# Optimization experiments

Hardware: AMD Instinct MI355X
Metric: run time of the kernel (lower is better)

## Reference

```python
import jax, jax.numpy as jnp
import numpy as np


def log_g(x):
    # log of g(x) = x+0.5 if x>=0 else sigmoid(x), computed stably
    return jnp.where(x >= 0, jnp.log(jax.nn.relu(x) + 0.5), -jax.nn.softplus(-x))


def setup_inputs() -> dict:
    key = jax.random.key(0)
    ks = jax.random.split(key, 6)
    B, S, D, H = 8, 4096, 1024, 1024
    scale = 1.0 / np.sqrt(D)
    return {
        "x": jax.random.normal(ks[0], (B, S, D), dtype=jnp.float32),
        "h0": jax.random.normal(ks[1], (B, 1, H), dtype=jnp.float32),
        "Wz": jax.random.normal(ks[2], (H, D), dtype=jnp.float32) * scale,
        "bz": jax.random.normal(ks[3], (H,), dtype=jnp.float32) * scale,
        "Wh": jax.random.normal(ks[4], (H, D), dtype=jnp.float32) * scale,
        "bh": jax.random.normal(ks[5], (H,), dtype=jnp.float32) * scale,
    }


def reference(x, h0, Wz, bz, Wh, bh):
    # x: (B,S,D), h0: (B,1,H)
    k = jnp.einsum("bsd,hd->bsh", x, Wz) + bz            # linear_z
    log_z = -jax.nn.softplus(-k)                          # log sigmoid(k)
    log_coeffs = -jax.nn.softplus(k)                      # log (1 - sigmoid(k))
    log_h0 = log_g(h0)                                    # (B,1,H)
    log_tilde_h = log_g(jnp.einsum("bsd,hd->bsh", x, Wh) + bh)
    log_values = jnp.concatenate([log_h0, log_z + log_tilde_h], axis=1)  # (B,S+1,H)
    a_star = jnp.pad(jnp.cumsum(log_coeffs, axis=1), ((0, 0), (1, 0), (0, 0)))  # (B,S+1,H)
    log_h0_plus_b_star = jax.lax.cumlogsumexp(log_values - a_star, axis=1)
    h = jnp.exp(a_star[:, 1:] + log_h0_plus_b_star[:, 1:])  # (B,S,H)
    return h
```

## Files before the change

### kernel.cpp

```cpp
#include <hip/hip_runtime.h>
#include <cstdint>
#include <cstddef>

#define B_  8
#define S_  4096
#define D_  1024
#define H_  1024
#define M_  (B_*S_)
#define NC_ 64
#define L_  (S_/NC_)

typedef __bf16 bf16x8 __attribute__((ext_vector_type(8)));
typedef float  f32x4  __attribute__((ext_vector_type(4)));
typedef uint16_t u16x8 __attribute__((ext_vector_type(8)));

__device__ __forceinline__ uint16_t f2bf(float f) {
  union { float f; uint32_t u; } v; v.f = f;
  uint32_t u = v.u;
  u += 0x7FFFu + ((u >> 16) & 1u);
  return (uint16_t)(u >> 16);
}
__device__ __forceinline__ float gfun(float x) {
  return x >= 0.0f ? x + 0.5f
                   : __builtin_amdgcn_rcpf(1.0f + __expf(-x));
}
__device__ __forceinline__ void unpack_cv(uint32_t u, float& c, float& v) {
  union { uint32_t u; _Float16 h[2]; } p; p.u = u;
  c = (float)p.h[0]; v = (float)p.h[1];
}

__global__ __launch_bounds__(256) void cvt_kernel(const float* __restrict__ in,
                                                  uint16_t* __restrict__ out,
                                                  int n8) {
  int i = blockIdx.x * 256 + threadIdx.x;
  if (i >= n8) return;
  const float4* p = (const float4*)in;
  float4 a = p[2 * i], b = p[2 * i + 1];
  u16x8 v;
  v[0] = f2bf(a.x); v[1] = f2bf(a.y); v[2] = f2bf(a.z); v[3] = f2bf(a.w);
  v[4] = f2bf(b.x); v[5] = f2bf(b.y); v[6] = f2bf(b.z); v[7] = f2bf(b.w);
  *(u16x8*)&out[8 * i] = v;
}

#define BM 128
#define BNH 64
#define BK 64
__global__ __launch_bounds__(256)
void fused_gemm_kernel(const uint16_t* __restrict__ A,
                       const uint16_t* __restrict__ Wz,
                       const uint16_t* __restrict__ Wh,
                       const float* __restrict__ bz,
                       const float* __restrict__ bh,
                       uint32_t* __restrict__ cv) {
  __shared__ __attribute__((aligned(16))) uint16_t As[BM * BK];
  __shared__ __attribute__((aligned(16))) uint16_t Bzs[BNH * BK];
  __shared__ __attribute__((aligned(16))) uint16_t Bhs[BNH * BK];
  const int tid  = threadIdx.x;
  const int lane = tid & 63;
  const int wave = tid >> 6;
  const int mTile = blockIdx.y * BM;
  const int nTile = blockIdx.x * BNH;
  const int wm0 = (wave >> 1) * 64;
  const int wn0 = (wave & 1) * 32;
  const int q  = lane >> 4;
  const int mn = lane & 15;

  f32x4 accK[4][2] = {};
  f32x4 accP[4][2] = {};

  for (int kt = 0; kt < D_; kt += BK) {
    __syncthreads();
    #pragma unroll
    for (int i = 0; i < 4; i++) {
      int u = i * 256 + tid;
      int r = u >> 3;
      int c = (u & 7) ^ (r & 7);
      __builtin_amdgcn_global_load_lds(
          (const __attribute__((address_space(1))) void*)(A + (size_t)(mTile + r) * D_ + kt + c * 8),
          (__attribute__((address_space(3))) void*)&As[(i * 256 + wave * 64) * 8],
          16, 0, 0);
    }
    #pragma unroll
    for (int i = 0; i < 2; i++) {
      int u = i * 256 + tid;
      int r = u >> 3;
      int c = (u & 7) ^ (r & 7);
      __builtin_amdgcn_global_load_lds(
          (const __attribute__((address_space(1))) void*)(Wz + (size_t)(nTile + r) * D_ + kt + c * 8),
          (__attribute__((address_space(3))) void*)&Bzs[(i * 256 + wave * 64) * 8],
          16, 0, 0);
    }
    #pragma unroll
    for (int i = 0; i < 2; i++) {
      int u = i * 256 + tid;
      int r = u >> 3;
      int c = (u & 7) ^ (r & 7);
      __builtin_amdgcn_global_load_lds(
          (const __attribute__((address_space(1))) void*)(Wh + (size_t)(nTile + r) * D_ + kt + c * 8),
          (__attribute__((address_space(3))) void*)&Bhs[(i * 256 + wave * 64) * 8],
          16, 0, 0);
    }
    __syncthreads();

    #pragma unroll
    for (int s = 0; s < 2; s++) {
      bf16x8 av[4], bzv[2], bhv[2];
      const int cu = s * 4 + q;
      #pragma unroll
      for (int tm = 0; tm < 4; tm++) {
        int r = wm0 + tm * 16 + mn;
        av[tm] = *(const bf16x8*)&As[(r * 8 + (cu ^ (r & 7))) * 8];
      }
      #pragma unroll
      for (int tn = 0; tn < 2; tn++) {
        int r = wn0 + tn * 16 + mn;
        int unit = r * 8 + (cu ^ (r & 7));
        bzv[tn] = *(const bf16x8*)&Bzs[unit * 8];
        bhv[tn] = *(const bf16x8*)&Bhs[unit * 8];
      }
      #pragma unroll
      for (int tm = 0; tm < 4; tm++)
        #pragma unroll
        for (int tn = 0; tn < 2; tn++) {
          accK[tm][tn] = __builtin_amdgcn_mfma_f32_16x16x32_bf16(
              av[tm], bzv[tn], accK[tm][tn], 0, 0, 0);
          accP[tm][tn] = __builtin_amdgcn_mfma_f32_16x16x32_bf16(
              av[tm], bhv[tn], accP[tm][tn], 0, 0, 0);
        }
    }
  }

  #pragma unroll
  for (int tn = 0; tn < 2; tn++) {
    int col = nTile + wn0 + tn * 16 + mn;
    float bzc = bz[col], bhc = bh[col];
    #pragma unroll
    for (int tm = 0; tm < 4; tm++) {
      int row0 = mTile + wm0 + tm * 16 + q * 4;
      #pragma unroll
      for (int i = 0; i < 4; i++) {
        float kv = accK[tm][tn][i] + bzc;
        float pv = accP[tm][tn][i] + bhc;
        float c = __builtin_amdgcn_rcpf(1.0f + __expf(kv));
        float z = 1.0f - c;
        float v = z * gfun(pv);
        union { _Float16 h[2]; uint32_t u; } pk;
        pk.h[0] = (_Float16)c; pk.h[1] = (_Float16)v;
        cv[(size_t)(row0 + i) * H_ + col] = pk.u;
      }
    }
  }
}

__global__ __launch_bounds__(256) void scan_chunk_kernel(
    const uint32_t* __restrict__ cv, float4* __restrict__ Cc,
    float4* __restrict__ Vc) {
  const int tid = threadIdx.x;
  const int nc = blockIdx.x, b = blockIdx.y;
  const uint4* cv4 = (const uint4*)cv;
  size_t base = (size_t)(b * S_ + nc * L_) * (H_ / 4) + tid;
  float C[4] = {1.f, 1.f, 1.f, 1.f};
  float V[4] = {0.f, 0.f, 0.f, 0.f};
  #pragma unroll 4
  for (int t = 0; t < L_; t++) {
    uint4 w = cv4[base + (size_t)t * (H_ / 4)];
    float c, v;
    unpack_cv(w.x, c, v); C[0] *= c; V[0] = c * V[0] + v;
    unpack_cv(w.y, c, v); C[1] *= c; V[1] = c * V[1] + v;
    unpack_cv(w.z, c, v); C[2] *= c; V[2] = c * V[2] + v;
    unpack_cv(w.w, c, v); C[3] *= c; V[3] = c * V[3] + v;
  }
  size_t o = (size_t)(b * NC_ + nc) * (H_ / 4) + tid;
  Cc[o] = (float4){C[0], C[1], C[2], C[3]};
  Vc[o] = (float4){V[0], V[1], V[2], V[3]};
}

__global__ __launch_bounds__(256) void chunk_prefix_kernel(
    const float* __restrict__ Cc, const float* __restrict__ Vc,
    const float* __restrict__ h0, float* __restrict__ Hin) {
  int h = blockIdx.x * 256 + threadIdx.x;
  int b = blockIdx.y;
  float Hv = gfun(h0[(size_t)b * H_ + h]);
  Hin[(size_t)(b * NC_) * H_ + h] = Hv;
  #pragma unroll 8
  for (int nc = 1; nc < NC_; nc++) {
    size_t idx = (size_t)(b * NC_ + nc - 1) * H_ + h;
    Hv = Cc[idx] * Hv + Vc[idx];
    Hin[(size_t)(b * NC_ + nc) * H_ + h] = Hv;
  }
}

__global__ __launch_bounds__(256) void scan_apply_kernel(
    const uint32_t* __restrict__ cv, const float4* __restrict__ Hin,
    float4* __restrict__ out) {
  const int tid = threadIdx.x;
  const int nc = blockIdx.x, b = blockIdx.y;
  const uint4* cv4 = (const uint4*)cv;
  size_t base = (size_t)(b * S_ + nc * L_) * (H_ / 4) + tid;
  float4 Hq = Hin[(size_t)(b * NC_ + nc) * (H_ / 4) + tid];
  float Hr[4] = {Hq.x, Hq.y, Hq.z, Hq.w};
  #pragma unroll 4
  for (int t = 0; t < L_; t++) {
    size_t idx = base + (size_t)t * (H_ / 4);
    uint4 w = cv4[idx];
    float c, v;
    unpack_cv(w.x, c, v); Hr[0] = c * Hr[0] + v;
    unpack_cv(w.y, c, v); Hr[1] = c * Hr[1] + v;
    unpack_cv(w.z, c, v); Hr[2] = c * Hr[2] + v;
    unpack_cv(w.w, c, v); Hr[3] = c * Hr[3] + v;
    out[idx] = (float4){Hr[0], Hr[1], Hr[2], Hr[3]};
  }
}

extern "C" void kernel_launch(void* const* d_in, const int* in_sizes, int n_in,
                              void* d_out, int out_size, void* d_ws, size_t ws_size,
                              hipStream_t stream) {
  const float* x  = (const float*)d_in[0];
  const float* h0 = (const float*)d_in[1];
  const float* Wz = (const float*)d_in[2];
  const float* bz = (const float*)d_in[3];
  const float* Wh = (const float*)d_in[4];
  const float* bh = (const float*)d_in[5];
  float* out = (float*)d_out;

  char* ws = (char*)d_ws;
  uint16_t* xb  = (uint16_t*)ws; ws += (size_t)M_ * D_ * 2;
  uint16_t* Wzb = (uint16_t*)ws; ws += (size_t)H_ * D_ * 2;
  uint16_t* Whb = (uint16_t*)ws; ws += (size_t)H_ * D_ * 2;
  uint32_t* cvb = (uint32_t*)ws; ws += (size_t)M_ * H_ * 4;
  char* alias = (char*)xb;
  float* Cc  = (float*)alias; alias += (size_t)B_ * NC_ * H_ * 4;
  float* Vc  = (float*)alias; alias += (size_t)B_ * NC_ * H_ * 4;
  float* Hin = (float*)alias; alias += (size_t)B_ * NC_ * H_ * 4;

  cvt_kernel<<<dim3(M_ * D_ / 8 / 256), 256, 0, stream>>>(x, xb, M_ * D_ / 8);
  cvt_kernel<<<dim3(H_ * D_ / 8 / 256), 256, 0, stream>>>(Wz, Wzb, H_ * D_ / 8);
  cvt_kernel<<<dim3(H_ * D_ / 8 / 256), 256, 0, stream>>>(Wh, Whb, H_ * D_ / 8);

  fused_gemm_kernel<<<dim3(H_ / BNH, M_ / BM), 256, 0, stream>>>(
      xb, Wzb, Whb, bz, bh, cvb);

  scan_chunk_kernel<<<dim3(NC_, B_), 256, 0, stream>>>(cvb, (float4*)Cc, (float4*)Vc);
  chunk_prefix_kernel<<<dim3(H_ / 256, B_), 256, 0, stream>>>(Cc, Vc, h0, Hin);
  scan_apply_kernel<<<dim3(NC_, B_), 256, 0, stream>>>(cvb, (const float4*)Hin, (float4*)out);
}
```

Measured before the change: 481.7 us.

## Enlarge GEMM N tile, merge conversion kernels, fold chunk prefix into apply

The GEMM tile width per block doubles to 128 columns, so each wave computes 4x4 MFMA tiles for both weight matrices, with precomputed load pointers and a two-blocks-per-CU launch bound. The goal is more reuse of each loaded A tile and fewer blocks. The three fp32-to-bf16 conversion launches become one grid-stride kernel. The serial chunk-prefix kernel is removed and each apply block recomputes its own incoming state from the chunk summaries, trading redundant prefix work for one fewer launch and no Hin buffer. The larger accumulator set raises register pressure and may lower occupancy.

```diff
diff --git a/kernel.cpp b/kernel.cpp
--- a/kernel.cpp
+++ b/kernel.cpp
@@ -29,23 +29,31 @@
   c = (float)p.h[0]; v = (float)p.h[1];
 }
 
-__global__ __launch_bounds__(256) void cvt_kernel(const float* __restrict__ in,
-                                                  uint16_t* __restrict__ out,
-                                                  int n8) {
-  int i = blockIdx.x * 256 + threadIdx.x;
-  if (i >= n8) return;
-  const float4* p = (const float4*)in;
-  float4 a = p[2 * i], b = p[2 * i + 1];
-  u16x8 v;
-  v[0] = f2bf(a.x); v[1] = f2bf(a.y); v[2] = f2bf(a.z); v[3] = f2bf(a.w);
-  v[4] = f2bf(b.x); v[5] = f2bf(b.y); v[6] = f2bf(b.z); v[7] = f2bf(b.w);
-  *(u16x8*)&out[8 * i] = v;
+#define X8_  (M_ * D_ / 8)
+#define W8_  (H_ * D_ / 8)
+#define TOT8_ (X8_ + 2 * W8_)
+__global__ __launch_bounds__(256) void cvt_all_kernel(
+    const float* __restrict__ x, const float* __restrict__ Wz,
+    const float* __restrict__ Wh, uint16_t* __restrict__ xb,
+    uint16_t* __restrict__ Wzb, uint16_t* __restrict__ Whb) {
+  int stride = gridDim.x * 256;
+  for (int u = blockIdx.x * 256 + threadIdx.x; u < TOT8_; u += stride) {
+    const float* src; uint16_t* dst;
+    if (u < X8_)            { src = x  + (size_t)u * 8;          dst = xb  + (size_t)u * 8; }
+    else if (u < X8_ + W8_) { size_t v = u - X8_;        src = Wz + v * 8; dst = Wzb + v * 8; }
+    else                    { size_t v = u - X8_ - W8_;  src = Wh + v * 8; dst = Whb + v * 8; }
+    float4 a = ((const float4*)src)[0], b = ((const float4*)src)[1];
+    u16x8 o;
+    o[0] = f2bf(a.x); o[1] = f2bf(a.y); o[2] = f2bf(a.z); o[3] = f2bf(a.w);
+    o[4] = f2bf(b.x); o[5] = f2bf(b.y); o[6] = f2bf(b.z); o[7] = f2bf(b.w);
+    *(u16x8*)dst = o;
+  }
 }
 
 #define BM 128
-#define BNH 64
+#define BNH 128
 #define BK 64
-__global__ __launch_bounds__(256)
+__global__ __launch_bounds__(256, 2)
 void fused_gemm_kernel(const uint16_t* __restrict__ A,
                        const uint16_t* __restrict__ Wz,
                        const uint16_t* __restrict__ Wh,
@@ -61,50 +69,49 @@
   const int mTile = blockIdx.y * BM;
   const int nTile = blockIdx.x * BNH;
   const int wm0 = (wave >> 1) * 64;
-  const int wn0 = (wave & 1) * 32;
+  const int wn0 = (wave & 1) * 64;
   const int q  = lane >> 4;
   const int mn = lane & 15;
 
-  f32x4 accK[4][2] = {};
-  f32x4 accP[4][2] = {};
+  const uint16_t* aPtr[4];
+  const uint16_t* zPtr[4];
+  const uint16_t* hPtr[4];
+  #pragma unroll
+  for (int i = 0; i < 4; i++) {
+    int u = i * 256 + tid;
+    int r = u >> 3;
+    int c = (u & 7) ^ (r & 7);
+    aPtr[i] = A  + (size_t)(mTile + r) * D_ + c * 8;
+    zPtr[i] = Wz + (size_t)(nTile + r) * D_ + c * 8;
+    hPtr[i] = Wh + (size_t)(nTile + r) * D_ + c * 8;
+  }
+  const int ldsDst = (wave * 64 + lane) * 8;
+
+  f32x4 accK[4][4] = {};
+  f32x4 accP[4][4] = {};
 
   for (int kt = 0; kt < D_; kt += BK) {
     __syncthreads();
     #pragma unroll
-    for (int i = 0; i < 4; i++) {
-      int u = i * 256 + tid;
-      int r = u >> 3;
-      int c = (u & 7) ^ (r & 7);
+    for (int i = 0; i < 4; i++)
       __builtin_amdgcn_global_load_lds(
-          (const __attribute__((address_space(1))) void*)(A + (size_t)(mTile + r) * D_ + kt + c * 8),
-          (__attribute__((address_space(3))) void*)&As[(i * 256 + wave * 64) * 8],
-          16, 0, 0);
-    }
-    #pragma unroll
-    for (int i = 0; i < 2; i++) {
-      int u = i * 256 + tid;
-      int r = u >> 3;
-      int c = (u & 7) ^ (r & 7);
+          (const __attribute__((address_space(1))) void*)(aPtr[i] + kt),
+          (__attribute__((address_space(3))) void*)&As[i * 2048 + ldsDst], 16, 0, 0);
+    #pragma unroll
+    for (int i = 0; i < 4; i++)
       __builtin_amdgcn_global_load_lds(
-          (const __attribute__((address_space(1))) void*)(Wz + (size_t)(nTile + r) * D_ + kt + c * 8),
-          (__attribute__((address_space(3))) void*)&Bzs[(i * 256 + wave * 64) * 8],
-          16, 0, 0);
-    }
-    #pragma unroll
-    for (int i = 0; i < 2; i++) {
-      int u = i * 256 + tid;
-      int r = u >> 3;
-      int c = (u & 7) ^ (r & 7);
+          (const __attribute__((address_space(1))) void*)(zPtr[i] + kt),
+          (__attribute__((address_space(3))) void*)&Bzs[i * 2048 + ldsDst], 16, 0, 0);
+    #pragma unroll
+    for (int i = 0; i < 4; i++)
       __builtin_amdgcn_global_load_lds(
-          (const __attribute__((address_space(1))) void*)(Wh + (size_t)(nTile + r) * D_ + kt + c * 8),
-          (__attribute__((address_space(3))) void*)&Bhs[(i * 256 + wave * 64) * 8],
-          16, 0, 0);
-    }
+          (const __attribute__((address_space(1))) void*)(hPtr[i] + kt),
+          (__attribute__((address_space(3))) void*)&Bhs[i * 2048 + ldsDst], 16, 0, 0);
     __syncthreads();
 
     #pragma unroll
     for (int s = 0; s < 2; s++) {
-      bf16x8 av[4], bzv[2], bhv[2];
+      bf16x8 av[4], bzv[4], bhv[4];
       const int cu = s * 4 + q;
       #pragma unroll
       for (int tm = 0; tm < 4; tm++) {
@@ -112,7 +119,7 @@
         av[tm] = *(const bf16x8*)&As[(r * 8 + (cu ^ (r & 7))) * 8];
       }
       #pragma unroll
-      for (int tn = 0; tn < 2; tn++) {
+      for (int tn = 0; tn < 4; tn++) {
         int r = wn0 + tn * 16 + mn;
         int unit = r * 8 + (cu ^ (r & 7));
         bzv[tn] = *(const bf16x8*)&Bzs[unit * 8];
@@ -121,7 +128,7 @@
       #pragma unroll
       for (int tm = 0; tm < 4; tm++)
         #pragma unroll
-        for (int tn = 0; tn < 2; tn++) {
+        for (int tn = 0; tn < 4; tn++) {
           accK[tm][tn] = __builtin_amdgcn_mfma_f32_16x16x32_bf16(
               av[tm], bzv[tn], accK[tm][tn], 0, 0, 0);
           accP[tm][tn] = __builtin_amdgcn_mfma_f32_16x16x32_bf16(
@@ -131,7 +138,7 @@
   }
 
   #pragma unroll
-  for (int tn = 0; tn < 2; tn++) {
+  for (int tn = 0; tn < 4; tn++) {
     int col = nTile + wn0 + tn * 16 + mn;
     float bzc = bz[col], bhc = bh[col];
     #pragma unroll
@@ -175,30 +182,28 @@
   Vc[o] = (float4){V[0], V[1], V[2], V[3]};
 }
 
-__global__ __launch_bounds__(256) void chunk_prefix_kernel(
-    const float* __restrict__ Cc, const float* __restrict__ Vc,
-    const float* __restrict__ h0, float* __restrict__ Hin) {
-  int h = blockIdx.x * 256 + threadIdx.x;
-  int b = blockIdx.y;
-  float Hv = gfun(h0[(size_t)b * H_ + h]);
-  Hin[(size_t)(b * NC_) * H_ + h] = Hv;
-  #pragma unroll 8
-  for (int nc = 1; nc < NC_; nc++) {
-    size_t idx = (size_t)(b * NC_ + nc - 1) * H_ + h;
-    Hv = Cc[idx] * Hv + Vc[idx];
-    Hin[(size_t)(b * NC_ + nc) * H_ + h] = Hv;
-  }
-}
-
 __global__ __launch_bounds__(256) void scan_apply_kernel(
-    const uint32_t* __restrict__ cv, const float4* __restrict__ Hin,
+    const uint32_t* __restrict__ cv, const float4* __restrict__ Cc,
+    const float4* __restrict__ Vc, const float* __restrict__ h0,
     float4* __restrict__ out) {
   const int tid = threadIdx.x;
   const int nc = blockIdx.x, b = blockIdx.y;
   const uint4* cv4 = (const uint4*)cv;
+
+  float Hr[4];
+  #pragma unroll
+  for (int j = 0; j < 4; j++) Hr[j] = gfun(h0[(size_t)b * H_ + tid * 4 + j]);
+  #pragma unroll 4
+  for (int j = 0; j < nc; j++) {
+    size_t idx = (size_t)(b * NC_ + j) * (H_ / 4) + tid;
+    float4 Cq = Cc[idx], Vq = Vc[idx];
+    Hr[0] = Cq.x * Hr[0] + Vq.x;
+    Hr[1] = Cq.y * Hr[1] + Vq.y;
+    Hr[2] = Cq.z * Hr[2] + Vq.z;
+    Hr[3] = Cq.w * Hr[3] + Vq.w;
+  }
+
   size_t base = (size_t)(b * S_ + nc * L_) * (H_ / 4) + tid;
-  float4 Hq = Hin[(size_t)(b * NC_ + nc) * (H_ / 4) + tid];
-  float Hr[4] = {Hq.x, Hq.y, Hq.z, Hq.w};
   #pragma unroll 4
   for (int t = 0; t < L_; t++) {
     size_t idx = base + (size_t)t * (H_ / 4);
@@ -231,16 +236,13 @@
   char* alias = (char*)xb;
   float* Cc  = (float*)alias; alias += (size_t)B_ * NC_ * H_ * 4;
   float* Vc  = (float*)alias; alias += (size_t)B_ * NC_ * H_ * 4;
-  float* Hin = (float*)alias; alias += (size_t)B_ * NC_ * H_ * 4;
-
-  cvt_kernel<<<dim3(M_ * D_ / 8 / 256), 256, 0, stream>>>(x, xb, M_ * D_ / 8);
-  cvt_kernel<<<dim3(H_ * D_ / 8 / 256), 256, 0, stream>>>(Wz, Wzb, H_ * D_ / 8);
-  cvt_kernel<<<dim3(H_ * D_ / 8 / 256), 256, 0, stream>>>(Wh, Whb, H_ * D_ / 8);
+
+  cvt_all_kernel<<<dim3(2048), 256, 0, stream>>>(x, Wz, Wh, xb, Wzb, Whb);
 
   fused_gemm_kernel<<<dim3(H_ / BNH, M_ / BM), 256, 0, stream>>>(
       xb, Wzb, Whb, bz, bh, cvb);
 
   scan_chunk_kernel<<<dim3(NC_, B_), 256, 0, stream>>>(cvb, (float4*)Cc, (float4*)Vc);
-  chunk_prefix_kernel<<<dim3(H_ / 256, B_), 256, 0, stream>>>(Cc, Vc, h0, Hin);
-  scan_apply_kernel<<<dim3(NC_, B_), 256, 0, stream>>>(cvb, (const float4*)Hin, (float4*)out);
-}
+  scan_apply_kernel<<<dim3(NC_, B_), 256, 0, stream>>>(
+      cvb, (const float4*)Cc, (const float4*)Vc, h0, (float4*)out);
+}
```

Measured after the change: 442.6 us. 8.1% less time.
